# Kernel tuning notes

Hardware: AMD Instinct MI355X
Metric: run time of the kernel (lower is better)

## Reference

```python
import jax, jax.numpy as jnp
import numpy as np
from jax import lax
from jax.scipy.special import logsumexp

TEMP_MIN, TEMP_MAX = 0.1, 1.0
B, I, J, C = 2, 128, 512, 256


def setup_inputs() -> dict:
    key = jax.random.key(0)
    k1, k2, k3 = jax.random.split(key, 3)
    return {
        "text_embeddings": jax.random.normal(k1, (B, I, C), dtype=jnp.float32),
        "mel_embeddings": jax.random.normal(k2, (B, J, C), dtype=jnp.float32),
        "text_mask": jnp.ones((B, I), dtype=jnp.float32),
        "mel_mask": jnp.ones((B, J), dtype=jnp.float32),
        "noise": jax.random.gumbel(k3, (B, I, J), dtype=jnp.float32),  # -log(-log(U))
        "temperature_ratio": jnp.float32(0.5),
    }


def _cond_prob(energy, text_mask, mel_mask, direction):
    # energy: [B, I, J]; returns [B, I, J, K] log conditional probs (normalized over axis 2)
    b, i, j = energy.shape
    if direction == "alpha":
        k = j
        tri = jnp.arange(j)[:, None] >= jnp.arange(k)[None, :]  # triu(ones(J,J)).T layout -> j >= k
        mel_k = mel_mask
    else:  # beta
        k = j - 1
        tri = jnp.arange(j)[:, None] <= jnp.arange(k)[None, :]  # tril(ones(J-1,J)).T layout -> j <= k
        mel_k = mel_mask[:, :k]
    valid = (
        (text_mask[:, :, None, None] * mel_mask[:, None, :, None] * mel_k[:, None, None, :]) > 0
    ) & tri[None, None]
    e4 = jnp.where(valid, energy[..., None], -jnp.inf)  # [B,I,J,K]
    e4 = e4 - logsumexp(e4, axis=2, keepdims=True)
    return jnp.where(valid, e4, jnp.asarray(-10.0, energy.dtype))


def reference(text_embeddings, mel_embeddings, text_mask, mel_mask, noise, temperature_ratio):
    b, i_len, ct = text_embeddings.shape
    j_len, cm = mel_embeddings.shape[1], mel_embeddings.shape[2]
    ninf = jnp.asarray(-jnp.inf, text_embeddings.dtype)

    energy = jnp.einsum("bic,bjc->bij", text_embeddings, mel_embeddings) / np.sqrt(ct * cm)
    temperature = TEMP_MIN + (TEMP_MAX - TEMP_MIN) * temperature_ratio
    energy = (energy + noise) / temperature

    cpa = _cond_prob(energy, text_mask, mel_mask, "alpha")  # [B,I,J,J]
    cpb = _cond_prob(energy, text_mask, mel_mask, "beta")   # [B,I,J,J-1]

    # forward (alpha) recursion over text dim: alpha[:, i, j+1] = LSE_k(alpha[:, i-1, k] + cpa[:, i-1, j, k])
    init_a = jnp.full((b, j_len + 1), -jnp.inf, energy.dtype).at[:, 0].set(0.0)

    def astep(carry, cpa_i):  # carry [B, J+1], cpa_i [B, J, J]
        row = logsumexp(carry[:, None, :-1] + cpa_i, axis=2)  # [B, J]
        new = jnp.concatenate([jnp.full((b, 1), -jnp.inf, energy.dtype), row], axis=1)
        return new, row

    _, arows = lax.scan(astep, init_a, jnp.swapaxes(cpa, 0, 1))
    alpha = jnp.swapaxes(arows, 0, 1)  # [B, I, J] == alpha[:, 1:, 1:]

    # backward (beta) recursion: beta[:, i, j] = LSE_k(beta[:, i+1, k+1] + cpb[:, i, j, k])
    init_b = jnp.full((b, j_len), -jnp.inf, energy.dtype).at[:, -1].set(0.0)

    def bstep(carry, cpb_i):  # carry [B, J], cpb_i [B, J, J-1]
        row = logsumexp(carry[:, None, 1:] + cpb_i, axis=2)
        return row, row

    _, brows = lax.scan(bstep, init_b, jnp.flip(jnp.swapaxes(cpb[:, : i_len - 1], 0, 1), axis=0))
    beta = jnp.concatenate([jnp.flip(brows, axis=0), init_b[None]], axis=0)
    beta = jnp.swapaxes(beta, 0, 1)  # [B, I, J]

    gamma = alpha + beta
    gmask = (text_mask[:, :, None] * mel_mask[:, None, :]) > 0
    gamma = jnp.where(gmask, gamma, ninf)
    gamma = jnp.where(gmask, gamma - logsumexp(gamma, axis=1, keepdims=True), ninf)

    expanded = jnp.einsum("bij,bic->bjc", jnp.exp(gamma), text_embeddings)
    expanded = expanded * mel_mask[:, :, None]
    return gamma, expanded
```

## Files before the change

### kernel.cpp

```cpp
#include <hip/hip_runtime.h>
#include <math.h>

#define BB 2
#define II 128
#define JJ 512
#define CC 256
#define NEL (BB*II*JJ)
#define NINF (-INFINITY)
#define K10 4.5399929762484854e-5f

template<int CTRL, int RM = 0xf, int BM = 0xf, bool BC = true>
__device__ __forceinline__ float dppf(float x) {
    return __int_as_float(__builtin_amdgcn_update_dpp(
        0, __float_as_int(x), CTRL, RM, BM, BC));
}
__device__ __forceinline__ float wscan_incl(float x) {
    x += dppf<0x111>(x);
    x += dppf<0x112>(x);
    x += dppf<0x114>(x);
    x += dppf<0x118>(x);
    x += dppf<0x142, 0xa>(x);
    x += dppf<0x143, 0xc>(x);
    return x;
}
__device__ __forceinline__ float lane_shr1(float x) { return dppf<0x138>(x); }
__device__ __forceinline__ float bcast63(float x) {
    return __int_as_float(__builtin_amdgcn_readlane(__float_as_int(x), 63));
}

__device__ __forceinline__ void loadrow8(const float* __restrict__ p, float v[8]) {
    float4 a = *reinterpret_cast<const float4*>(p);
    float4 b = *reinterpret_cast<const float4*>(p + 4);
    v[0]=a.x; v[1]=a.y; v[2]=a.z; v[3]=a.w;
    v[4]=b.x; v[5]=b.y; v[6]=b.z; v[7]=b.w;
}
__device__ __forceinline__ void loadrow8_rev(const float* __restrict__ row, int lane, float v[8]) {
    float t[8];
    loadrow8(row + 504 - 8 * lane, t);
    #pragma unroll
    for (int q = 0; q < 8; ++q) v[q] = t[7 - q];
}
__device__ __forceinline__ void storerow8(float* __restrict__ p, const float v[8]) {
    *reinterpret_cast<float4*>(p)     = make_float4(v[0],v[1],v[2],v[3]);
    *reinterpret_cast<float4*>(p + 4) = make_float4(v[4],v[5],v[6],v[7]);
}

__global__ __launch_bounds__(256) void energy_kernel(
        const float* __restrict__ text, const float* __restrict__ mel,
        const float* __restrict__ noise, const float* __restrict__ ratio,
        float* __restrict__ e) {
    __shared__ float melS[64][65];
    __shared__ float texS[8][65];
    int b  = blockIdx.x;
    int i0 = blockIdx.y * 8;
    int j0 = blockIdx.z * 64;
    int t = threadIdx.x;
    int jj = t & 63, ig = t >> 6;
    float acc0 = 0.f, acc1 = 0.f;
    for (int cc = 0; cc < CC; cc += 64) {
        #pragma unroll
        for (int k = 0; k < 4; ++k) {
            int idx = t + k * 256;
            int row = idx >> 4, seg = idx & 15;
            float4 v = *reinterpret_cast<const float4*>(
                mel + (size_t)(b * JJ + j0 + row) * CC + cc + seg * 4);
            melS[row][seg*4+0] = v.x; melS[row][seg*4+1] = v.y;
            melS[row][seg*4+2] = v.z; melS[row][seg*4+3] = v.w;
        }
        if (t < 128) {
            int row = t >> 4, seg = t & 15;
            float4 v = *reinterpret_cast<const float4*>(
                text + (size_t)(b * II + i0 + row) * CC + cc + seg * 4);
            texS[row][seg*4+0] = v.x; texS[row][seg*4+1] = v.y;
            texS[row][seg*4+2] = v.z; texS[row][seg*4+3] = v.w;
        }
        __syncthreads();
        #pragma unroll 8
        for (int c = 0; c < 64; ++c) {
            float m = melS[jj][c];
            acc0 = fmaf(m, texS[ig*2+0][c], acc0);
            acc1 = fmaf(m, texS[ig*2+1][c], acc1);
        }
        __syncthreads();
    }
    float temp = 0.1f + 0.9f * ratio[0];
    float rtmp = 1.0f / temp;
    int r0 = (b * II + i0 + ig*2 + 0) * JJ + j0 + jj;
    int r1 = (b * II + i0 + ig*2 + 1) * JJ + j0 + jj;
    e[r0] = (acc0 * (1.0f/256.0f) + noise[r0]) * rtmp;
    e[r1] = (acc1 * (1.0f/256.0f) + noise[r1]) * rtmp;
}

__global__ __launch_bounds__(64) void dscan_kernel(
        const float* __restrict__ e, float* __restrict__ Ee,
        float* __restrict__ Wa, float* __restrict__ Wb) {
    int row = blockIdx.x;
    int lane = threadIdx.x;
    float v[8];
    loadrow8(e + row * JJ + lane * 8, v);
    float m = v[0];
    #pragma unroll
    for (int q = 1; q < 8; ++q) m = fmaxf(m, v[q]);
    #pragma unroll
    for (int d = 1; d < 64; d <<= 1) m = fmaxf(m, __shfl_xor(m, d, 64));
    float x[8];
    #pragma unroll
    for (int q = 0; q < 8; ++q) x[q] = __expf(v[q] - m);
    storerow8(Ee + row * JJ + lane * 8, x);
    float run = 0.f, P[8];
    #pragma unroll
    for (int q = 0; q < 8; ++q) { run += x[q]; P[q] = run; }
    float sc = wscan_incl(run);
    float cp = lane_shr1(sc);
    float run2 = 0.f, S[8];
    #pragma unroll
    for (int q = 7; q >= 0; --q) { run2 += x[q]; S[q] = run2; }
    float sd = run2;
    #pragma unroll
    for (int d = 1; d < 64; d <<= 1) { float o = __shfl_down(sd, d, 64); sd += (lane + d < 64) ? o : 0.0f; }
    float cs = __shfl_down(sd, 1, 64); if (lane == 63) cs = 0.f;
    float wa[8], wb[8];
    #pragma unroll
    for (int q = 0; q < 8; ++q) {
        wa[q] = 1.0f / (S[q] + cs);
        wb[q] = 1.0f / (P[q] + cp);
    }
    storerow8(Wa + row * JJ + lane * 8, wa);
    storerow8(Wb + row * JJ + lane * 8, wb);
}

__device__ __forceinline__ void astep(
    int i, int lane, int base, int off, bool pf,
    float (&p)[8], float& c, float (&eb)[8], float (&wb)[8],
    const float* __restrict__ Ee, const float* __restrict__ Wa,
    float* __restrict__ pa, float* __restrict__ ca)
{
    float ein[8], win[8];
    #pragma unroll
    for (int q = 0; q < 8; ++q) { ein[q] = eb[q]; win[q] = wb[q]; }
    if (pf) {
        loadrow8(Ee + (base + i + 3) * JJ + off, eb);
        loadrow8(Wa + (base + i + 3) * JJ + off, wb);
    }
    float pup = lane_shr1(p[7]);
    float Y[8], Z[8];
    float run = pup * win[0];
    Y[0] = run;
    #pragma unroll
    for (int q = 1; q < 8; ++q) { run += p[q-1] * win[q]; Y[q] = run; }
    float z7 = (lane == 63) ? 0.0f : p[7];
    Z[0] = p[0];
    #pragma unroll
    for (int q = 1; q < 7; ++q) Z[q] = Z[q-1] + p[q];
    Z[7] = Z[6] + z7;
    float sy = wscan_incl(Y[7]);
    float sz = wscan_incl(Z[7]);
    float oy = lane_shr1(sy);
    float oz = lane_shr1(sz);
    float T  = fmaxf(bcast63(sz), 1e-30f);
    float rT = __builtin_amdgcn_rcpf(T);
    c += __logf(T);
    #pragma unroll
    for (int q = 0; q < 8; ++q) {
        float S1 = oy + Y[q];
        float zq = (q == 7) ? z7 : p[q];
        float S2 = fmaxf(T - (oz + Z[q]) + zq, 0.0f);
        p[q] = (ein[q] * S1 + K10 * S2) * rT;
    }
    storerow8(pa + (base + i) * JJ + off, p);
    if (lane == 0) ca[base + i] = c;
}

__device__ __forceinline__ void bstep(
    int i, int lane, int base, int off, bool pf,
    float (&p)[8], float& c, float (&eb)[8], float (&wb)[8],
    const float* __restrict__ Ee, const float* __restrict__ Wb,
    float* __restrict__ pb, float* __restrict__ cb)
{
    float ein[8], win[8];
    #pragma unroll
    for (int q = 0; q < 8; ++q) { ein[q] = eb[q]; win[q] = wb[q]; }
    if (pf) {
        loadrow8_rev(Ee + (base + i - 3) * JJ, lane, eb);
        loadrow8_rev(Wb + (base + i - 3) * JJ, lane, wb);
    }
    float pup = lane_shr1(p[7]);
    float W[8], N[8];
    float run = pup * win[0];
    W[0] = run;
    #pragma unroll
    for (int q = 1; q < 8; ++q) { run += p[q-1] * win[q]; W[q] = run; }
    N[0] = pup;
    #pragma unroll
    for (int q = 1; q < 8; ++q) N[q] = N[q-1] + p[q-1];
    float sw = wscan_incl(W[7]);
    float sn = wscan_incl(N[7]);
    float ow = lane_shr1(sw);
    float on = lane_shr1(sn);
    float T  = fmaxf(bcast63(sn), 1e-30f);
    float rT = __builtin_amdgcn_rcpf(T);
    c += __logf(T);
    #pragma unroll
    for (int q = 0; q < 8; ++q) {
        float QA = ow + W[q];
        float QB = fmaxf(T - (on + N[q]), 0.0f);
        p[q] = (ein[q] * QA + K10 * QB) * rT;
    }
    storerow8(pb + (base + i) * JJ + off, p);
    if (lane == 0) cb[base + i] = c;
}

__global__ __launch_bounds__(64) void scan_ab_kernel(
        const float* __restrict__ Ee, const float* __restrict__ Wa,
        const float* __restrict__ Wb,
        float* __restrict__ pa, float* __restrict__ pb,
        float* __restrict__ ca, float* __restrict__ cb) {
    int b = blockIdx.x >> 1, dir = blockIdx.x & 1;
    int lane = threadIdx.x;
    int base = b * II, off = lane * 8;
    float p[8], c = 0.0f;
    float b0e[8], b0w[8], b1e[8], b1w[8], b2e[8], b2w[8];

    if (dir == 0) {
        float e0[8];
        loadrow8(Ee + base * JJ + off, e0);
        float wa00 = Wa[base * JJ];
        #pragma unroll
        for (int q = 0; q < 8; ++q) p[q] = e0[q] * wa00;
        storerow8(pa + base * JJ + off, p);
        if (lane == 0) ca[base] = 0.0f;
        loadrow8(Ee + (base + 1) * JJ + off, b1e);
        loadrow8(Wa + (base + 1) * JJ + off, b1w);
        loadrow8(Ee + (base + 2) * JJ + off, b2e);
        loadrow8(Wa + (base + 2) * JJ + off, b2w);
        loadrow8(Ee + (base + 3) * JJ + off, b0e);
        loadrow8(Wa + (base + 3) * JJ + off, b0w);
        int i = 1;
        #pragma unroll 1
        for (; i + 2 <= II - 1; i += 3) {
            astep(i,     lane, base, off, i + 3 < II, p, c, b1e, b1w, Ee, Wa, pa, ca);
            astep(i + 1, lane, base, off, i + 4 < II, p, c, b2e, b2w, Ee, Wa, pa, ca);
            astep(i + 2, lane, base, off, i + 5 < II, p, c, b0e, b0w, Ee, Wa, pa, ca);
        }
        for (; i < II; ++i)
            astep(i, lane, base, off, false, p, c, b1e, b1w, Ee, Wa, pa, ca);
    } else {
        #pragma unroll
        for (int q = 0; q < 8; ++q) p[q] = 0.0f;
        p[0] = (lane == 0) ? 1.0f : 0.0f;
        storerow8(pb + (base + II - 1) * JJ + off, p);
        if (lane == 0) cb[base + II - 1] = 0.0f;
        loadrow8_rev(Ee + (base + II - 2) * JJ, lane, b0e);
        loadrow8_rev(Wb + (base + II - 2) * JJ, lane, b0w);
        loadrow8_rev(Ee + (base + II - 3) * JJ, lane, b2e);
        loadrow8_rev(Wb + (base + II - 3) * JJ, lane, b2w);
        loadrow8_rev(Ee + (base + II - 4) * JJ, lane, b1e);
        loadrow8_rev(Wb + (base + II - 4) * JJ, lane, b1w);
        int i = II - 2;
        #pragma unroll 1
        for (; i - 2 >= 0; i -= 3) {
            bstep(i,     lane, base, off, i - 3 >= 0, p, c, b0e, b0w, Ee, Wb, pb, cb);
            bstep(i - 1, lane, base, off, i - 4 >= 0, p, c, b2e, b2w, Ee, Wb, pb, cb);
            bstep(i - 2, lane, base, off, i - 5 >= 0, p, c, b1e, b1w, Ee, Wb, pb, cb);
        }
        for (; i >= 0; --i)
            bstep(i, lane, base, off, false, p, c, b0e, b0w, Ee, Wb, pb, cb);
    }
}

__global__ __launch_bounds__(256) void gamma_kernel(
        const float* __restrict__ pa, const float* __restrict__ pb,
        const float* __restrict__ ca, const float* __restrict__ cb,
        float* __restrict__ gamma_out, float* __restrict__ wexp) {
    __shared__ float cas[II], cbs[II];
    __shared__ float Ms[4][64], Ss[4][64];
    int b  = blockIdx.x >> 3;
    int jt = blockIdx.x & 7;
    int t = threadIdx.x;
    int jl = t & 63, ic = t >> 6;
    int jj = jt * 64 + jl;
    for (int i = t; i < II; i += 256) { cas[i] = ca[b*II + i]; cbs[i] = cb[b*II + i]; }
    __syncthreads();
    int idx0  = b * II * JJ + jj;
    int idx0r = b * II * JJ + (JJ - 1 - jj);
    float M = NINF, S = 0.f;
    #pragma unroll 4
    for (int k = 0; k < 32; ++k) {
        int i = ic * 32 + k;
        float g = __logf(pa[idx0 + i*JJ]) + cas[i] + __logf(pb[idx0r + i*JJ]) + cbs[i];
        float Mn = fmaxf(M, g);
        if (Mn != NINF) { S = S * __expf(M - Mn) + __expf(g - Mn); M = Mn; }
    }
    Ms[ic][jl] = M; Ss[ic][jl] = S;
    __syncthreads();
    float M2 = Ms[0][jl], S2 = Ss[0][jl];
    #pragma unroll
    for (int k = 1; k < 4; ++k) {
        float m = Ms[k][jl], s = Ss[k][jl];
        float Mn = fmaxf(M2, m);
        if (Mn != NINF) { S2 = S2 * __expf(M2 - Mn) + s * __expf(m - Mn); M2 = Mn; }
    }
    float L = (M2 == NINF) ? -1e30f : (M2 + __logf(S2));
    #pragma unroll 4
    for (int k = 0; k < 32; ++k) {
        int i = ic * 32 + k;
        float g = __logf(pa[idx0 + i*JJ]) + cas[i] + __logf(pb[idx0r + i*JJ]) + cbs[i];
        float gn = g - L;
        gamma_out[idx0 + i*JJ] = fmaxf(gn, -1e30f);
        wexp[idx0 + i*JJ] = __expf(gn);
    }
}

__global__ __launch_bounds__(512) void expand_kernel(
        const float* __restrict__ wexp, const float* __restrict__ text,
        const float* __restrict__ mmask, float* __restrict__ outx) {
    __shared__ float wt[II][8];
    __shared__ float part[256][9];
    const int nJT = JJ / 8;
    int b = blockIdx.x / nJT;
    int jj0 = (blockIdx.x % nJT) * 8;
    int t = threadIdx.x;
    int c = t & 255, half = t >> 8;
    for (int idx = t; idx < II * 8; idx += 512) {
        int i = idx >> 3, q = idx & 7;
        wt[i][q] = wexp[(b*II + i)*JJ + jj0 + q];
    }
    __syncthreads();
    float acc[8] = {0,0,0,0,0,0,0,0};
    #pragma unroll 4
    for (int k = 0; k < 64; ++k) {
        int i = half * 64 + k;
        float tv = text[(b*II + i)*CC + c];
        #pragma unroll
        for (int q = 0; q < 8; ++q) acc[q] = fmaf(wt[i][q], tv, acc[q]);
    }
    if (half == 1) {
        #pragma unroll
        for (int q = 0; q < 8; ++q) part[c][q] = acc[q];
    }
    __syncthreads();
    if (half == 0) {
        #pragma unroll
        for (int q = 0; q < 8; ++q) {
            outx[(b*JJ + jj0 + q)*CC + c] =
                (acc[q] + part[c][q]) * mmask[b*JJ + jj0 + q];
        }
    }
}

extern "C" void kernel_launch(void* const* d_in, const int* in_sizes, int n_in,
                              void* d_out, int out_size, void* d_ws, size_t ws_size,
                              hipStream_t stream) {
    const float* text  = (const float*)d_in[0];
    const float* mel   = (const float*)d_in[1];
    const float* mmask = (const float*)d_in[3];
    const float* noise = (const float*)d_in[4];
    const float* ratio = (const float*)d_in[5];
    float* gamma_out = (float*)d_out;
    float* expanded  = (float*)d_out + NEL;

    float* ws = (float*)d_ws;
    float* Ee = ws;
    float* Wa = ws +   NEL;
    float* Wb = ws + 2*NEL;
    float* pa = ws + 3*NEL;
    float* pb = ws + 4*NEL;
    float* ca = ws + 5*NEL;
    float* cb = ws + 5*NEL + BB*II;
    float* e    = pa;
    float* wexp = Wa;

    hipLaunchKernelGGL(energy_kernel, dim3(BB, II/8, JJ/64), dim3(256), 0, stream,
                       text, mel, noise, ratio, e);
    hipLaunchKernelGGL(dscan_kernel, dim3(BB*II), dim3(64), 0, stream, e, Ee, Wa, Wb);
    hipLaunchKernelGGL(scan_ab_kernel, dim3(BB*2), dim3(64), 0, stream,
                       Ee, Wa, Wb, pa, pb, ca, cb);
    hipLaunchKernelGGL(gamma_kernel, dim3(BB*8), dim3(256), 0, stream,
                       pa, pb, ca, cb, gamma_out, wexp);
    hipLaunchKernelGGL(expand_kernel, dim3(BB*(JJ/8)), dim3(512), 0, stream,
                       wexp, text, mmask, expanded);
}
```

Baseline: 140.8 us.

## Interleave both batches per scan wavefront and compute gamma in linear domain

The alpha/beta scan kernel now runs one wavefront per direction that processes both batch items together. The two independent recurrences are interleaved so their DPP scans and loads can hide each other's latency, and the prefetch depth drops from three rows ahead to two. The gamma kernel replaces the per-element log/online-max softmax with a linear-domain product pa*pb*exp(ca+cb-max), normalised by a plain sum. That removes most transcendental calls, at the risk of underflow or precision loss in the normalisation.

```diff
diff --git a/kernel.cpp b/kernel.cpp
--- a/kernel.cpp
+++ b/kernel.cpp
@@ -129,85 +129,105 @@
     storerow8(Wb + row * JJ + lane * 8, wb);
 }
 
-__device__ __forceinline__ void astep(
-    int i, int lane, int base, int off, bool pf,
-    float (&p)[8], float& c, float (&eb)[8], float (&wb)[8],
+__device__ __forceinline__ void astep_dual(
+    int i, int lane, int off, bool pf,
+    float (&p)[2][8], float (&c)[2],
+    float (&CE)[2][8], float (&CW)[2][8],
+    float (&LE)[2][8], float (&LW)[2][8],
     const float* __restrict__ Ee, const float* __restrict__ Wa,
     float* __restrict__ pa, float* __restrict__ ca)
 {
-    float ein[8], win[8];
-    #pragma unroll
-    for (int q = 0; q < 8; ++q) { ein[q] = eb[q]; win[q] = wb[q]; }
     if (pf) {
-        loadrow8(Ee + (base + i + 3) * JJ + off, eb);
-        loadrow8(Wa + (base + i + 3) * JJ + off, wb);
-    }
-    float pup = lane_shr1(p[7]);
-    float Y[8], Z[8];
-    float run = pup * win[0];
-    Y[0] = run;
-    #pragma unroll
-    for (int q = 1; q < 8; ++q) { run += p[q-1] * win[q]; Y[q] = run; }
-    float z7 = (lane == 63) ? 0.0f : p[7];
-    Z[0] = p[0];
-    #pragma unroll
-    for (int q = 1; q < 7; ++q) Z[q] = Z[q-1] + p[q];
-    Z[7] = Z[6] + z7;
-    float sy = wscan_incl(Y[7]);
-    float sz = wscan_incl(Z[7]);
-    float oy = lane_shr1(sy);
-    float oz = lane_shr1(sz);
-    float T  = fmaxf(bcast63(sz), 1e-30f);
-    float rT = __builtin_amdgcn_rcpf(T);
-    c += __logf(T);
-    #pragma unroll
-    for (int q = 0; q < 8; ++q) {
-        float S1 = oy + Y[q];
-        float zq = (q == 7) ? z7 : p[q];
-        float S2 = fmaxf(T - (oz + Z[q]) + zq, 0.0f);
-        p[q] = (ein[q] * S1 + K10 * S2) * rT;
-    }
-    storerow8(pa + (base + i) * JJ + off, p);
-    if (lane == 0) ca[base + i] = c;
-}
-
-__device__ __forceinline__ void bstep(
-    int i, int lane, int base, int off, bool pf,
-    float (&p)[8], float& c, float (&eb)[8], float (&wb)[8],
+        #pragma unroll
+        for (int h = 0; h < 2; ++h) {
+            loadrow8(Ee + (size_t)(h*II + i + 2) * JJ + off, LE[h]);
+            loadrow8(Wa + (size_t)(h*II + i + 2) * JJ + off, LW[h]);
+        }
+    }
+    float pup[2], z7[2], Y[2][8], Z[2][8];
+    #pragma unroll
+    for (int h = 0; h < 2; ++h) pup[h] = lane_shr1(p[h][7]);
+    #pragma unroll
+    for (int h = 0; h < 2; ++h) {
+        float run = pup[h] * CW[h][0];
+        Y[h][0] = run;
+        #pragma unroll
+        for (int q = 1; q < 8; ++q) { run += p[h][q-1] * CW[h][q]; Y[h][q] = run; }
+        z7[h] = (lane == 63) ? 0.0f : p[h][7];
+        Z[h][0] = p[h][0];
+        #pragma unroll
+        for (int q = 1; q < 7; ++q) Z[h][q] = Z[h][q-1] + p[h][q];
+        Z[h][7] = Z[h][6] + z7[h];
+    }
+    float sy[2], sz[2];
+    #pragma unroll
+    for (int h = 0; h < 2; ++h) { sy[h] = wscan_incl(Y[h][7]); sz[h] = wscan_incl(Z[h][7]); }
+    #pragma unroll
+    for (int h = 0; h < 2; ++h) {
+        float oy = lane_shr1(sy[h]);
+        float oz = lane_shr1(sz[h]);
+        float T  = fmaxf(bcast63(sz[h]), 1e-30f);
+        float rT = __builtin_amdgcn_rcpf(T);
+        c[h] += __logf(T);
+        #pragma unroll
+        for (int q = 0; q < 8; ++q) {
+            float S1 = oy + Y[h][q];
+            float zq = (q == 7) ? z7[h] : p[h][q];
+            float S2 = fmaxf(T - (oz + Z[h][q]) + zq, 0.0f);
+            p[h][q] = (CE[h][q] * S1 + K10 * S2) * rT;
+        }
+        storerow8(pa + (size_t)(h*II + i) * JJ + off, p[h]);
+    }
+    if (lane == 0) { ca[i] = c[0]; ca[II + i] = c[1]; }
+}
+
+__device__ __forceinline__ void bstep_dual(
+    int i, int lane, int off, bool pf,
+    float (&p)[2][8], float (&c)[2],
+    float (&CE)[2][8], float (&CW)[2][8],
+    float (&LE)[2][8], float (&LW)[2][8],
     const float* __restrict__ Ee, const float* __restrict__ Wb,
     float* __restrict__ pb, float* __restrict__ cb)
 {
-    float ein[8], win[8];
-    #pragma unroll
-    for (int q = 0; q < 8; ++q) { ein[q] = eb[q]; win[q] = wb[q]; }
     if (pf) {
-        loadrow8_rev(Ee + (base + i - 3) * JJ, lane, eb);
-        loadrow8_rev(Wb + (base + i - 3) * JJ, lane, wb);
-    }
-    float pup = lane_shr1(p[7]);
-    float W[8], N[8];
-    float run = pup * win[0];
-    W[0] = run;
-    #pragma unroll
-    for (int q = 1; q < 8; ++q) { run += p[q-1] * win[q]; W[q] = run; }
-    N[0] = pup;
-    #pragma unroll
-    for (int q = 1; q < 8; ++q) N[q] = N[q-1] + p[q-1];
-    float sw = wscan_incl(W[7]);
-    float sn = wscan_incl(N[7]);
-    float ow = lane_shr1(sw);
-    float on = lane_shr1(sn);
-    float T  = fmaxf(bcast63(sn), 1e-30f);
-    float rT = __builtin_amdgcn_rcpf(T);
-    c += __logf(T);
-    #pragma unroll
-    for (int q = 0; q < 8; ++q) {
-        float QA = ow + W[q];
-        float QB = fmaxf(T - (on + N[q]), 0.0f);
-        p[q] = (ein[q] * QA + K10 * QB) * rT;
-    }
-    storerow8(pb + (base + i) * JJ + off, p);
-    if (lane == 0) cb[base + i] = c;
+        #pragma unroll
+        for (int h = 0; h < 2; ++h) {
+            loadrow8_rev(Ee + (size_t)(h*II + i - 2) * JJ, lane, LE[h]);
+            loadrow8_rev(Wb + (size_t)(h*II + i - 2) * JJ, lane, LW[h]);
+        }
+    }
+    float pup[2], W[2][8], N[2][8];
+    #pragma unroll
+    for (int h = 0; h < 2; ++h) pup[h] = lane_shr1(p[h][7]);
+    #pragma unroll
+    for (int h = 0; h < 2; ++h) {
+        float run = pup[h] * CW[h][0];
+        W[h][0] = run;
+        #pragma unroll
+        for (int q = 1; q < 8; ++q) { run += p[h][q-1] * CW[h][q]; W[h][q] = run; }
+        N[h][0] = pup[h];
+        #pragma unroll
+        for (int q = 1; q < 8; ++q) N[h][q] = N[h][q-1] + p[h][q-1];
+    }
+    float sw[2], sn[2];
+    #pragma unroll
+    for (int h = 0; h < 2; ++h) { sw[h] = wscan_incl(W[h][7]); sn[h] = wscan_incl(N[h][7]); }
+    #pragma unroll
+    for (int h = 0; h < 2; ++h) {
+        float ow = lane_shr1(sw[h]);
+        float on = lane_shr1(sn[h]);
+        float T  = fmaxf(bcast63(sn[h]), 1e-30f);
+        float rT = __builtin_amdgcn_rcpf(T);
+        c[h] += __logf(T);
+        #pragma unroll
+        for (int q = 0; q < 8; ++q) {
+            float QA = ow + W[h][q];
+            float QB = fmaxf(T - (on + N[h][q]), 0.0f);
+            p[h][q] = (CE[h][q] * QA + K10 * QB) * rT;
+        }
+        storerow8(pb + (size_t)(h*II + i) * JJ + off, p[h]);
+    }
+    if (lane == 0) { cb[i] = c[0]; cb[II + i] = c[1]; }
 }
 
 __global__ __launch_bounds__(64) void scan_ab_kernel(
@@ -215,56 +235,64 @@
         const float* __restrict__ Wb,
         float* __restrict__ pa, float* __restrict__ pb,
         float* __restrict__ ca, float* __restrict__ cb) {
-    int b = blockIdx.x >> 1, dir = blockIdx.x & 1;
+    int dir = blockIdx.x;
     int lane = threadIdx.x;
-    int base = b * II, off = lane * 8;
-    float p[8], c = 0.0f;
-    float b0e[8], b0w[8], b1e[8], b1w[8], b2e[8], b2w[8];
+    int off = lane * 8;
+    float p[2][8], c[2] = {0.0f, 0.0f};
+    float b0e[2][8], b0w[2][8], b1e[2][8], b1w[2][8], b2e[2][8], b2w[2][8];
 
     if (dir == 0) {
-        float e0[8];
-        loadrow8(Ee + base * JJ + off, e0);
-        float wa00 = Wa[base * JJ];
-        #pragma unroll
-        for (int q = 0; q < 8; ++q) p[q] = e0[q] * wa00;
-        storerow8(pa + base * JJ + off, p);
-        if (lane == 0) ca[base] = 0.0f;
-        loadrow8(Ee + (base + 1) * JJ + off, b1e);
-        loadrow8(Wa + (base + 1) * JJ + off, b1w);
-        loadrow8(Ee + (base + 2) * JJ + off, b2e);
-        loadrow8(Wa + (base + 2) * JJ + off, b2w);
-        loadrow8(Ee + (base + 3) * JJ + off, b0e);
-        loadrow8(Wa + (base + 3) * JJ + off, b0w);
+        #pragma unroll
+        for (int h = 0; h < 2; ++h) {
+            float e0[8];
+            loadrow8(Ee + (size_t)(h*II) * JJ + off, e0);
+            float wa00 = Wa[(size_t)(h*II) * JJ];
+            #pragma unroll
+            for (int q = 0; q < 8; ++q) p[h][q] = e0[q] * wa00;
+            storerow8(pa + (size_t)(h*II) * JJ + off, p[h]);
+        }
+        if (lane == 0) { ca[0] = 0.0f; ca[II] = 0.0f; }
+        #pragma unroll
+        for (int h = 0; h < 2; ++h) {
+            loadrow8(Ee + (size_t)(h*II + 1) * JJ + off, b1e[h]);
+            loadrow8(Wa + (size_t)(h*II + 1) * JJ + off, b1w[h]);
+            loadrow8(Ee + (size_t)(h*II + 2) * JJ + off, b2e[h]);
+            loadrow8(Wa + (size_t)(h*II + 2) * JJ + off, b2w[h]);
+        }
         int i = 1;
         #pragma unroll 1
         for (; i + 2 <= II - 1; i += 3) {
-            astep(i,     lane, base, off, i + 3 < II, p, c, b1e, b1w, Ee, Wa, pa, ca);
-            astep(i + 1, lane, base, off, i + 4 < II, p, c, b2e, b2w, Ee, Wa, pa, ca);
-            astep(i + 2, lane, base, off, i + 5 < II, p, c, b0e, b0w, Ee, Wa, pa, ca);
+            astep_dual(i,   lane, off, i+2 < II, p, c, b1e, b1w, b0e, b0w, Ee, Wa, pa, ca);
+            astep_dual(i+1, lane, off, i+3 < II, p, c, b2e, b2w, b1e, b1w, Ee, Wa, pa, ca);
+            astep_dual(i+2, lane, off, i+4 < II, p, c, b0e, b0w, b2e, b2w, Ee, Wa, pa, ca);
         }
         for (; i < II; ++i)
-            astep(i, lane, base, off, false, p, c, b1e, b1w, Ee, Wa, pa, ca);
+            astep_dual(i, lane, off, false, p, c, b1e, b1w, b0e, b0w, Ee, Wa, pa, ca);
     } else {
         #pragma unroll
-        for (int q = 0; q < 8; ++q) p[q] = 0.0f;
-        p[0] = (lane == 0) ? 1.0f : 0.0f;
-        storerow8(pb + (base + II - 1) * JJ + off, p);
-        if (lane == 0) cb[base + II - 1] = 0.0f;
-        loadrow8_rev(Ee + (base + II - 2) * JJ, lane, b0e);
-        loadrow8_rev(Wb + (base + II - 2) * JJ, lane, b0w);
-        loadrow8_rev(Ee + (base + II - 3) * JJ, lane, b2e);
-        loadrow8_rev(Wb + (base + II - 3) * JJ, lane, b2w);
-        loadrow8_rev(Ee + (base + II - 4) * JJ, lane, b1e);
-        loadrow8_rev(Wb + (base + II - 4) * JJ, lane, b1w);
+        for (int h = 0; h < 2; ++h) {
+            #pragma unroll
+            for (int q = 0; q < 8; ++q) p[h][q] = 0.0f;
+            p[h][0] = (lane == 0) ? 1.0f : 0.0f;
+            storerow8(pb + (size_t)(h*II + II - 1) * JJ + off, p[h]);
+        }
+        if (lane == 0) { cb[II - 1] = 0.0f; cb[II + II - 1] = 0.0f; }
+        #pragma unroll
+        for (int h = 0; h < 2; ++h) {
+            loadrow8_rev(Ee + (size_t)(h*II + II - 2) * JJ, lane, b0e[h]);
+            loadrow8_rev(Wb + (size_t)(h*II + II - 2) * JJ, lane, b0w[h]);
+            loadrow8_rev(Ee + (size_t)(h*II + II - 3) * JJ, lane, b2e[h]);
+            loadrow8_rev(Wb + (size_t)(h*II + II - 3) * JJ, lane, b2w[h]);
+        }
         int i = II - 2;
         #pragma unroll 1
         for (; i - 2 >= 0; i -= 3) {
-            bstep(i,     lane, base, off, i - 3 >= 0, p, c, b0e, b0w, Ee, Wb, pb, cb);
-            bstep(i - 1, lane, base, off, i - 4 >= 0, p, c, b2e, b2w, Ee, Wb, pb, cb);
-            bstep(i - 2, lane, base, off, i - 5 >= 0, p, c, b1e, b1w, Ee, Wb, pb, cb);
+            bstep_dual(i,   lane, off, i-2 >= 0, p, c, b0e, b0w, b1e, b1w, Ee, Wb, pb, cb);
+            bstep_dual(i-1, lane, off, i-3 >= 0, p, c, b2e, b2w, b0e, b0w, Ee, Wb, pb, cb);
+            bstep_dual(i-2, lane, off, i-4 >= 0, p, c, b1e, b1w, b2e, b2w, Ee, Wb, pb, cb);
         }
         for (; i >= 0; --i)
-            bstep(i, lane, base, off, false, p, c, b0e, b0w, Ee, Wb, pb, cb);
+            bstep_dual(i, lane, off, false, p, c, b0e, b0w, b1e, b1w, Ee, Wb, pb, cb);
     }
 }
 
@@ -272,42 +300,38 @@
         const float* __restrict__ pa, const float* __restrict__ pb,
         const float* __restrict__ ca, const float* __restrict__ cb,
         float* __restrict__ gamma_out, float* __restrict__ wexp) {
-    __shared__ float cas[II], cbs[II];
-    __shared__ float Ms[4][64], Ss[4][64];
+    __shared__ float sS[II], Ei[II];
+    __shared__ float Ds[4][64];
     int b  = blockIdx.x >> 3;
     int jt = blockIdx.x & 7;
     int t = threadIdx.x;
     int jl = t & 63, ic = t >> 6;
     int jj = jt * 64 + jl;
-    for (int i = t; i < II; i += 256) { cas[i] = ca[b*II + i]; cbs[i] = cb[b*II + i]; }
+    if (t < II) sS[t] = ca[b*II + t] + cb[b*II + t];
+    __syncthreads();
+    float maxc = sS[0];
+    #pragma unroll 8
+    for (int i = 1; i < II; ++i) maxc = fmaxf(maxc, sS[i]);
+    if (t < II) Ei[t] = __expf(sS[t] - maxc);
     __syncthreads();
     int idx0  = b * II * JJ + jj;
     int idx0r = b * II * JJ + (JJ - 1 - jj);
-    float M = NINF, S = 0.f;
+    float d = 0.f;
     #pragma unroll 4
     for (int k = 0; k < 32; ++k) {
         int i = ic * 32 + k;
-        float g = __logf(pa[idx0 + i*JJ]) + cas[i] + __logf(pb[idx0r + i*JJ]) + cbs[i];
-        float Mn = fmaxf(M, g);
-        if (Mn != NINF) { S = S * __expf(M - Mn) + __expf(g - Mn); M = Mn; }
-    }
-    Ms[ic][jl] = M; Ss[ic][jl] = S;
+        d = fmaf(pa[idx0 + i*JJ] * pb[idx0r + i*JJ], Ei[i], d);
+    }
+    Ds[ic][jl] = d;
     __syncthreads();
-    float M2 = Ms[0][jl], S2 = Ss[0][jl];
-    #pragma unroll
-    for (int k = 1; k < 4; ++k) {
-        float m = Ms[k][jl], s = Ss[k][jl];
-        float Mn = fmaxf(M2, m);
-        if (Mn != NINF) { S2 = S2 * __expf(M2 - Mn) + s * __expf(m - Mn); M2 = Mn; }
-    }
-    float L = (M2 == NINF) ? -1e30f : (M2 + __logf(S2));
+    float D = Ds[0][jl] + Ds[1][jl] + Ds[2][jl] + Ds[3][jl];
+    float rD = 1.0f / fmaxf(D, 1e-37f);
     #pragma unroll 4
     for (int k = 0; k < 32; ++k) {
         int i = ic * 32 + k;
-        float g = __logf(pa[idx0 + i*JJ]) + cas[i] + __logf(pb[idx0r + i*JJ]) + cbs[i];
-        float gn = g - L;
-        gamma_out[idx0 + i*JJ] = fmaxf(gn, -1e30f);
-        wexp[idx0 + i*JJ] = __expf(gn);
+        float P = pa[idx0 + i*JJ] * pb[idx0r + i*JJ] * Ei[i] * rD;
+        wexp[idx0 + i*JJ] = P;
+        gamma_out[idx0 + i*JJ] = fmaxf(__logf(P), -1e30f);
     }
 }
 
@@ -373,7 +397,7 @@
     hipLaunchKernelGGL(energy_kernel, dim3(BB, II/8, JJ/64), dim3(256), 0, stream,
                        text, mel, noise, ratio, e);
     hipLaunchKernelGGL(dscan_kernel, dim3(BB*II), dim3(64), 0, stream, e, Ee, Wa, Wb);
-    hipLaunchKernelGGL(scan_ab_kernel, dim3(BB*2), dim3(64), 0, stream,
+    hipLaunchKernelGGL(scan_ab_kernel, dim3(2), dim3(64), 0, stream,
                        Ee, Wa, Wb, pa, pb, ca, cb);
     hipLaunchKernelGGL(gamma_kernel, dim3(BB*8), dim3(256), 0, stream,
                        pa, pb, ca, cb, gamma_out, wexp);
```

Measured after the change: 171.7 us. 1.22x slower.

## Defer scan normalization, use tree prefix sums, and linear-domain gamma

Applied to the files above, without the earlier changes.

The alpha/beta scans now normalize only every fourth step and use log-depth tree prefix sums instead of serial running sums, shortening the dependency chain on the critical path. Row stores move to the start of the next step, and the prefetch depth grows to four buffers. The gamma kernel computes in the linear domain, weighting pa*pb by a per-row exp(ca+cb-max) and normalizing by the column sum. This removes most logs and exps and the online max-rescaling. The trade-off is a risk of overflow or underflow from unnormalized intermediates and from the linear-domain product.

```diff
diff --git a/kernel.cpp b/kernel.cpp
--- a/kernel.cpp
+++ b/kernel.cpp
@@ -26,6 +26,20 @@
 __device__ __forceinline__ float lane_shr1(float x) { return dppf<0x138>(x); }
 __device__ __forceinline__ float bcast63(float x) {
     return __int_as_float(__builtin_amdgcn_readlane(__float_as_int(x), 63));
+}
+
+__device__ __forceinline__ void tree_prefix8(const float x[8], float P[8]) {
+    float t[8];
+    t[0] = x[0];
+    #pragma unroll
+    for (int q = 1; q < 8; ++q) t[q] = x[q] + x[q-1];
+    float u[8];
+    u[0] = t[0]; u[1] = t[1];
+    #pragma unroll
+    for (int q = 2; q < 8; ++q) u[q] = t[q] + t[q-2];
+    P[0] = u[0]; P[1] = u[1]; P[2] = u[2]; P[3] = u[3];
+    #pragma unroll
+    for (int q = 4; q < 8; ++q) P[q] = u[q] + u[q-4];
 }
 
 __device__ __forceinline__ void loadrow8(const float* __restrict__ p, float v[8]) {
@@ -129,85 +143,99 @@
     storerow8(Wb + row * JJ + lane * 8, wb);
 }
 
+template<bool NORM>
 __device__ __forceinline__ void astep(
-    int i, int lane, int base, int off, bool pf,
-    float (&p)[8], float& c, float (&eb)[8], float (&wb)[8],
-    const float* __restrict__ Ee, const float* __restrict__ Wa,
-    float* __restrict__ pa, float* __restrict__ ca)
+    int i, int lane, int off, bool pf,
+    float (&p)[8], float& c,
+    float (&CE)[8], float (&CW)[8],
+    float (&LE)[8], float (&LW)[8],
+    const float* __restrict__ EeB, const float* __restrict__ WaB,
+    float* __restrict__ paB, float* __restrict__ caB)
 {
-    float ein[8], win[8];
-    #pragma unroll
-    for (int q = 0; q < 8; ++q) { ein[q] = eb[q]; win[q] = wb[q]; }
     if (pf) {
-        loadrow8(Ee + (base + i + 3) * JJ + off, eb);
-        loadrow8(Wa + (base + i + 3) * JJ + off, wb);
-    }
+        loadrow8(EeB + (size_t)(i + 3) * JJ + off, LE);
+        loadrow8(WaB + (size_t)(i + 3) * JJ + off, LW);
+    }
+    storerow8(paB + (size_t)(i - 1) * JJ + off, p);
+    if (lane == 0) caB[i - 1] = c;
+
     float pup = lane_shr1(p[7]);
+    float y[8];
+    y[0] = pup * CW[0];
+    #pragma unroll
+    for (int q = 1; q < 8; ++q) y[q] = p[q-1] * CW[q];
+    float zz[8];
+    #pragma unroll
+    for (int q = 0; q < 7; ++q) zz[q] = p[q];
+    zz[7] = (lane == 63) ? 0.0f : p[7];
     float Y[8], Z[8];
-    float run = pup * win[0];
-    Y[0] = run;
-    #pragma unroll
-    for (int q = 1; q < 8; ++q) { run += p[q-1] * win[q]; Y[q] = run; }
-    float z7 = (lane == 63) ? 0.0f : p[7];
-    Z[0] = p[0];
-    #pragma unroll
-    for (int q = 1; q < 7; ++q) Z[q] = Z[q-1] + p[q];
-    Z[7] = Z[6] + z7;
+    tree_prefix8(y, Y);
+    tree_prefix8(zz, Z);
     float sy = wscan_incl(Y[7]);
     float sz = wscan_incl(Z[7]);
     float oy = lane_shr1(sy);
     float oz = lane_shr1(sz);
-    float T  = fmaxf(bcast63(sz), 1e-30f);
-    float rT = __builtin_amdgcn_rcpf(T);
-    c += __logf(T);
+    float T  = bcast63(sz);
     #pragma unroll
     for (int q = 0; q < 8; ++q) {
         float S1 = oy + Y[q];
-        float zq = (q == 7) ? z7 : p[q];
-        float S2 = fmaxf(T - (oz + Z[q]) + zq, 0.0f);
-        p[q] = (ein[q] * S1 + K10 * S2) * rT;
-    }
-    storerow8(pa + (base + i) * JJ + off, p);
-    if (lane == 0) ca[base + i] = c;
-}
-
+        float S2 = fmaxf(T - (oz + Z[q]) + zz[q], 0.0f);
+        p[q] = fmaf(CE[q], S1, K10 * S2);
+    }
+    if (NORM) {
+        float Tc = fmaxf(T, 1e-30f);
+        float rT = __builtin_amdgcn_rcpf(Tc);
+        c += __logf(Tc);
+        #pragma unroll
+        for (int q = 0; q < 8; ++q) p[q] *= rT;
+    }
+}
+
+template<bool NORM>
 __device__ __forceinline__ void bstep(
-    int i, int lane, int base, int off, bool pf,
-    float (&p)[8], float& c, float (&eb)[8], float (&wb)[8],
-    const float* __restrict__ Ee, const float* __restrict__ Wb,
-    float* __restrict__ pb, float* __restrict__ cb)
+    int i, int lane, int off, bool pf,
+    float (&p)[8], float& c,
+    float (&CE)[8], float (&CW)[8],
+    float (&LE)[8], float (&LW)[8],
+    const float* __restrict__ EeB, const float* __restrict__ WbB,
+    float* __restrict__ pbB, float* __restrict__ cbB)
 {
-    float ein[8], win[8];
-    #pragma unroll
-    for (int q = 0; q < 8; ++q) { ein[q] = eb[q]; win[q] = wb[q]; }
     if (pf) {
-        loadrow8_rev(Ee + (base + i - 3) * JJ, lane, eb);
-        loadrow8_rev(Wb + (base + i - 3) * JJ, lane, wb);
-    }
+        loadrow8_rev(EeB + (size_t)(i - 3) * JJ, lane, LE);
+        loadrow8_rev(WbB + (size_t)(i - 3) * JJ, lane, LW);
+    }
+    storerow8(pbB + (size_t)(i + 1) * JJ + off, p);
+    if (lane == 0) cbB[i + 1] = c;
+
     float pup = lane_shr1(p[7]);
+    float pn[8];
+    pn[0] = pup;
+    #pragma unroll
+    for (int q = 1; q < 8; ++q) pn[q] = p[q-1];
+    float w[8];
+    #pragma unroll
+    for (int q = 0; q < 8; ++q) w[q] = pn[q] * CW[q];
     float W[8], N[8];
-    float run = pup * win[0];
-    W[0] = run;
-    #pragma unroll
-    for (int q = 1; q < 8; ++q) { run += p[q-1] * win[q]; W[q] = run; }
-    N[0] = pup;
-    #pragma unroll
-    for (int q = 1; q < 8; ++q) N[q] = N[q-1] + p[q-1];
+    tree_prefix8(w, W);
+    tree_prefix8(pn, N);
     float sw = wscan_incl(W[7]);
     float sn = wscan_incl(N[7]);
     float ow = lane_shr1(sw);
     float on = lane_shr1(sn);
-    float T  = fmaxf(bcast63(sn), 1e-30f);
-    float rT = __builtin_amdgcn_rcpf(T);
-    c += __logf(T);
+    float T  = bcast63(sn);
     #pragma unroll
     for (int q = 0; q < 8; ++q) {
         float QA = ow + W[q];
         float QB = fmaxf(T - (on + N[q]), 0.0f);
-        p[q] = (ein[q] * QA + K10 * QB) * rT;
-    }
-    storerow8(pb + (base + i) * JJ + off, p);
-    if (lane == 0) cb[base + i] = c;
+        p[q] = fmaf(CE[q], QA, K10 * QB);
+    }
+    if (NORM) {
+        float Tc = fmaxf(T, 1e-30f);
+        float rT = __builtin_amdgcn_rcpf(Tc);
+        c += __logf(Tc);
+        #pragma unroll
+        for (int q = 0; q < 8; ++q) p[q] *= rT;
+    }
 }
 
 __global__ __launch_bounds__(64) void scan_ab_kernel(
@@ -216,55 +244,57 @@
         float* __restrict__ pa, float* __restrict__ pb,
         float* __restrict__ ca, float* __restrict__ cb) {
     int b = blockIdx.x >> 1, dir = blockIdx.x & 1;
-    int lane = threadIdx.x;
-    int base = b * II, off = lane * 8;
+    int lane = threadIdx.x, off = lane * 8;
+    size_t base = (size_t)b * II * JJ;
     float p[8], c = 0.0f;
-    float b0e[8], b0w[8], b1e[8], b1w[8], b2e[8], b2w[8];
+    float B0e[8], B0w[8], B1e[8], B1w[8], B2e[8], B2w[8], B3e[8], B3w[8];
 
     if (dir == 0) {
+        const float* EeB = Ee + base; const float* WaB = Wa + base;
+        float* paB = pa + base; float* caB = ca + b * II;
+        loadrow8(EeB + (size_t)1*JJ + off, B1e); loadrow8(WaB + (size_t)1*JJ + off, B1w);
+        loadrow8(EeB + (size_t)2*JJ + off, B2e); loadrow8(WaB + (size_t)2*JJ + off, B2w);
+        loadrow8(EeB + (size_t)3*JJ + off, B3e); loadrow8(WaB + (size_t)3*JJ + off, B3w);
         float e0[8];
-        loadrow8(Ee + base * JJ + off, e0);
-        float wa00 = Wa[base * JJ];
+        loadrow8(EeB + off, e0);
+        float wa00 = WaB[0];
         #pragma unroll
         for (int q = 0; q < 8; ++q) p[q] = e0[q] * wa00;
-        storerow8(pa + base * JJ + off, p);
-        if (lane == 0) ca[base] = 0.0f;
-        loadrow8(Ee + (base + 1) * JJ + off, b1e);
-        loadrow8(Wa + (base + 1) * JJ + off, b1w);
-        loadrow8(Ee + (base + 2) * JJ + off, b2e);
-        loadrow8(Wa + (base + 2) * JJ + off, b2w);
-        loadrow8(Ee + (base + 3) * JJ + off, b0e);
-        loadrow8(Wa + (base + 3) * JJ + off, b0w);
         int i = 1;
         #pragma unroll 1
-        for (; i + 2 <= II - 1; i += 3) {
-            astep(i,     lane, base, off, i + 3 < II, p, c, b1e, b1w, Ee, Wa, pa, ca);
-            astep(i + 1, lane, base, off, i + 4 < II, p, c, b2e, b2w, Ee, Wa, pa, ca);
-            astep(i + 2, lane, base, off, i + 5 < II, p, c, b0e, b0w, Ee, Wa, pa, ca);
-        }
-        for (; i < II; ++i)
-            astep(i, lane, base, off, false, p, c, b1e, b1w, Ee, Wa, pa, ca);
+        for (; i + 3 <= II - 1; i += 4) {
+            astep<true >(i,   lane, off, i+3 < II, p, c, B1e,B1w, B0e,B0w, EeB,WaB,paB,caB);
+            astep<false>(i+1, lane, off, i+4 < II, p, c, B2e,B2w, B1e,B1w, EeB,WaB,paB,caB);
+            astep<false>(i+2, lane, off, i+5 < II, p, c, B3e,B3w, B2e,B2w, EeB,WaB,paB,caB);
+            astep<false>(i+3, lane, off, i+6 < II, p, c, B0e,B0w, B3e,B3w, EeB,WaB,paB,caB);
+        }
+        astep<true >(125, lane, off, false, p, c, B1e,B1w, B0e,B0w, EeB,WaB,paB,caB);
+        astep<false>(126, lane, off, false, p, c, B2e,B2w, B1e,B1w, EeB,WaB,paB,caB);
+        astep<false>(127, lane, off, false, p, c, B3e,B3w, B2e,B2w, EeB,WaB,paB,caB);
+        storerow8(paB + (size_t)127 * JJ + off, p);
+        if (lane == 0) caB[127] = c;
     } else {
+        const float* EeB = Ee + base; const float* WbB = Wb + base;
+        float* pbB = pb + base; float* cbB = cb + b * II;
+        loadrow8_rev(EeB + (size_t)126*JJ, lane, B2e); loadrow8_rev(WbB + (size_t)126*JJ, lane, B2w);
+        loadrow8_rev(EeB + (size_t)125*JJ, lane, B1e); loadrow8_rev(WbB + (size_t)125*JJ, lane, B1w);
+        loadrow8_rev(EeB + (size_t)124*JJ, lane, B0e); loadrow8_rev(WbB + (size_t)124*JJ, lane, B0w);
         #pragma unroll
         for (int q = 0; q < 8; ++q) p[q] = 0.0f;
         p[0] = (lane == 0) ? 1.0f : 0.0f;
-        storerow8(pb + (base + II - 1) * JJ + off, p);
-        if (lane == 0) cb[base + II - 1] = 0.0f;
-        loadrow8_rev(Ee + (base + II - 2) * JJ, lane, b0e);
-        loadrow8_rev(Wb + (base + II - 2) * JJ, lane, b0w);
-        loadrow8_rev(Ee + (base + II - 3) * JJ, lane, b2e);
-        loadrow8_rev(Wb + (base + II - 3) * JJ, lane, b2w);
-        loadrow8_rev(Ee + (base + II - 4) * JJ, lane, b1e);
-        loadrow8_rev(Wb + (base + II - 4) * JJ, lane, b1w);
         int i = II - 2;
         #pragma unroll 1
-        for (; i - 2 >= 0; i -= 3) {
-            bstep(i,     lane, base, off, i - 3 >= 0, p, c, b0e, b0w, Ee, Wb, pb, cb);
-            bstep(i - 1, lane, base, off, i - 4 >= 0, p, c, b2e, b2w, Ee, Wb, pb, cb);
-            bstep(i - 2, lane, base, off, i - 5 >= 0, p, c, b1e, b1w, Ee, Wb, pb, cb);
-        }
-        for (; i >= 0; --i)
-            bstep(i, lane, base, off, false, p, c, b0e, b0w, Ee, Wb, pb, cb);
+        for (; i - 3 >= 0; i -= 4) {
+            bstep<true >(i,   lane, off, i-3 >= 0, p, c, B2e,B2w, B3e,B3w, EeB,WbB,pbB,cbB);
+            bstep<false>(i-1, lane, off, i-4 >= 0, p, c, B1e,B1w, B2e,B2w, EeB,WbB,pbB,cbB);
+            bstep<false>(i-2, lane, off, i-5 >= 0, p, c, B0e,B0w, B1e,B1w, EeB,WbB,pbB,cbB);
+            bstep<false>(i-3, lane, off, i-6 >= 0, p, c, B3e,B3w, B0e,B0w, EeB,WbB,pbB,cbB);
+        }
+        bstep<true >(2, lane, off, false, p, c, B2e,B2w, B3e,B3w, EeB,WbB,pbB,cbB);
+        bstep<false>(1, lane, off, false, p, c, B1e,B1w, B2e,B2w, EeB,WbB,pbB,cbB);
+        bstep<false>(0, lane, off, false, p, c, B0e,B0w, B1e,B1w, EeB,WbB,pbB,cbB);
+        storerow8(pbB + off, p);
+        if (lane == 0) cbB[0] = c;
     }
 }
 
@@ -272,42 +302,38 @@
         const float* __restrict__ pa, const float* __restrict__ pb,
         const float* __restrict__ ca, const float* __restrict__ cb,
         float* __restrict__ gamma_out, float* __restrict__ wexp) {
-    __shared__ float cas[II], cbs[II];
-    __shared__ float Ms[4][64], Ss[4][64];
+    __shared__ float sS[II], Ei[II];
+    __shared__ float Ds[4][64];
     int b  = blockIdx.x >> 3;
     int jt = blockIdx.x & 7;
     int t = threadIdx.x;
     int jl = t & 63, ic = t >> 6;
     int jj = jt * 64 + jl;
-    for (int i = t; i < II; i += 256) { cas[i] = ca[b*II + i]; cbs[i] = cb[b*II + i]; }
+    if (t < II) sS[t] = ca[b*II + t] + cb[b*II + t];
+    __syncthreads();
+    float maxc = sS[0];
+    #pragma unroll 8
+    for (int i = 1; i < II; ++i) maxc = fmaxf(maxc, sS[i]);
+    if (t < II) Ei[t] = __expf(sS[t] - maxc);
     __syncthreads();
     int idx0  = b * II * JJ + jj;
     int idx0r = b * II * JJ + (JJ - 1 - jj);
-    float M = NINF, S = 0.f;
+    float d = 0.f;
     #pragma unroll 4
     for (int k = 0; k < 32; ++k) {
         int i = ic * 32 + k;
-        float g = __logf(pa[idx0 + i*JJ]) + cas[i] + __logf(pb[idx0r + i*JJ]) + cbs[i];
-        float Mn = fmaxf(M, g);
-        if (Mn != NINF) { S = S * __expf(M - Mn) + __expf(g - Mn); M = Mn; }
-    }
-    Ms[ic][jl] = M; Ss[ic][jl] = S;
+        d = fmaf(pa[idx0 + i*JJ] * pb[idx0r + i*JJ], Ei[i], d);
+    }
+    Ds[ic][jl] = d;
     __syncthreads();
-    float M2 = Ms[0][jl], S2 = Ss[0][jl];
-    #pragma unroll
-    for (int k = 1; k < 4; ++k) {
-        float m = Ms[k][jl], s = Ss[k][jl];
-        float Mn = fmaxf(M2, m);
-        if (Mn != NINF) { S2 = S2 * __expf(M2 - Mn) + s * __expf(m - Mn); M2 = Mn; }
-    }
-    float L = (M2 == NINF) ? -1e30f : (M2 + __logf(S2));
+    float D = Ds[0][jl] + Ds[1][jl] + Ds[2][jl] + Ds[3][jl];
+    float rD = 1.0f / fmaxf(D, 1e-37f);
     #pragma unroll 4
     for (int k = 0; k < 32; ++k) {
         int i = ic * 32 + k;
-        float g = __logf(pa[idx0 + i*JJ]) + cas[i] + __logf(pb[idx0r + i*JJ]) + cbs[i];
-        float gn = g - L;
-        gamma_out[idx0 + i*JJ] = fmaxf(gn, -1e30f);
-        wexp[idx0 + i*JJ] = __expf(gn);
+        float P = pa[idx0 + i*JJ] * pb[idx0r + i*JJ] * Ei[i] * rD;
+        wexp[idx0 + i*JJ] = P;
+        gamma_out[idx0 + i*JJ] = fmaxf(__logf(P), -1e30f);
     }
 }
 
```

Result: no change. 140.5 us (-0.3%).
